# Kernel optimization log

Hardware: AMD Instinct MI355X
Metric: run time of the kernel (lower is better)

Reference implementation:

```python
import jax, jax.numpy as jnp
import numpy as np

B, N, C = 1, 768, 384
H, P = 12, 4
DP = 128  # dim_pair
HP3 = H * P * 3  # 144


def linear(x, W, b):
    # torch nn.Linear: y = x @ W.T + b, W shape (out, in)
    return jnp.einsum('...i,oi->...o', x, W) + b


def setup_inputs() -> dict:
    key = jax.random.key(0)
    ks = jax.random.split(key, 24)
    w = lambda k, *s: jax.random.normal(k, s, jnp.float32) * 0.02
    inp = {
        'single': jax.random.normal(ks[0], (B, N, C), jnp.float32),
        'pair': jax.random.normal(ks[1], (B, N, N, DP), jnp.float32),
        'rot': jax.random.normal(ks[2], (B, N, 3, 3), jnp.float32),
        'trans': jax.random.normal(ks[3], (B, N, 3), jnp.float32),
        'Wq': w(ks[4], C, C), 'bq': jnp.zeros((C,), jnp.float32),
        'Wk': w(ks[5], C, C), 'bk': jnp.zeros((C,), jnp.float32),
        'Wv': w(ks[6], C, C), 'bv': jnp.zeros((C,), jnp.float32),
        'Wpb': w(ks[7], H, DP), 'bpb': jnp.zeros((H,), jnp.float32),
        'Wqp': w(ks[8], HP3, C), 'bqp': jnp.zeros((HP3,), jnp.float32),
        'Wkp': w(ks[9], HP3, C), 'bkp': jnp.zeros((HP3,), jnp.float32),
        'Wvp': w(ks[10], HP3, C), 'bvp': jnp.zeros((HP3,), jnp.float32),
        'Wo': w(ks[11], C, C), 'bo': jnp.zeros((C,), jnp.float32),
        'Wpo': w(ks[12], C, HP3), 'bpo': jnp.zeros((C,), jnp.float32),
        'ln_w': jnp.ones((C,), jnp.float32), 'ln_b': jnp.zeros((C,), jnp.float32),
    }
    return inp


def reference(single, pair, rot, trans, Wq, bq, Wk, bk, Wv, bv, Wpb, bpb,
              Wqp, bqp, Wkp, bkp, Wvp, bvp, Wo, bo, Wpo, bpo, ln_w, ln_b):
    Ch = C // H
    scale = Ch ** -0.5
    q = linear(single, Wq, bq).reshape(B, N, H, Ch)
    k = linear(single, Wk, bk).reshape(B, N, H, Ch)
    v = linear(single, Wv, bv).reshape(B, N, H, Ch)
    pair_bias = jnp.transpose(linear(pair, Wpb, bpb), (0, 3, 1, 2))  # (B,H,N,N)

    q_pts = linear(single, Wqp, bqp).reshape(B, N, H, P, 3)
    k_pts = linear(single, Wkp, bkp).reshape(B, N, H, P, 3)
    v_pts = linear(single, Wvp, bvp).reshape(B, N, H, P, 3)
    t = trans[:, :, None, None, :]  # (B,N,1,1,3)
    # rotate local points into global frame: p @ R + t
    q_g = jnp.einsum('bnhpd,bnde->bnhpe', q_pts, rot) + t
    k_g = jnp.einsum('bnhpd,bnde->bnhpe', k_pts, rot) + t
    v_g = jnp.einsum('bnhpd,bnde->bnhpe', v_pts, rot) + t

    q2 = jnp.sum(q_g ** 2, axis=(3, 4))  # (B,N,H)
    k2 = jnp.sum(k_g ** 2, axis=(3, 4))
    qk = jnp.einsum('bnhpd,bmhpd->bhnm', q_g, k_g)
    q2h = jnp.transpose(q2, (0, 2, 1))  # (B,H,N)
    k2h = jnp.transpose(k2, (0, 2, 1))
    point_logits = -0.5 * (q2h[..., :, None] + k2h[..., None, :] - 2.0 * qk) * scale
    scalar_logits = jnp.einsum('bnhc,bmhc->bhnm', q, k) * scale
    attn = jax.nn.softmax(scalar_logits + pair_bias + point_logits, axis=-1)

    weighted_scalar = jnp.einsum('bhnm,bmhc->bnhc', attn, v).reshape(B, N, C)
    weighted_points = jnp.einsum('bhnm,bmhpd->bnhpd', attn, v_g).reshape(B, N, HP3)
    point_proj = linear(weighted_points, Wpo, bpo)
    out = linear(weighted_scalar + point_proj, Wo, bo)

    x = single + out
    mu = jnp.mean(x, axis=-1, keepdims=True)
    var = jnp.mean((x - mu) ** 2, axis=-1, keepdims=True)
    return (x - mu) / jnp.sqrt(var + 1e-5) * ln_w + ln_b
```

## Files before the change

### kernel.cpp

```cpp
#include <hip/hip_runtime.h>
#include <math.h>

#define NRES 768
#define CDIM 384
#define HEADS 12
#define SCALE 0.17677669529663687f

typedef _Float16 f16;
typedef _Float16 __attribute__((ext_vector_type(8))) f16x8;
typedef float __attribute__((ext_vector_type(4))) f32x4;

__global__ __launch_bounds__(256) void prep_kernel(
    const float* __restrict__ Wq, const float* __restrict__ Wk, const float* __restrict__ Wv,
    const float* __restrict__ Wqp, const float* __restrict__ Wkp, const float* __restrict__ Wvp,
    const float* __restrict__ bq, const float* __restrict__ bk, const float* __restrict__ bv,
    const float* __restrict__ bqp, const float* __restrict__ bkp, const float* __restrict__ bvp,
    const float* __restrict__ single, const float* __restrict__ Wpo, const float* __restrict__ bpo,
    const float* __restrict__ Wo,
    f16* __restrict__ WcatH, float* __restrict__ bcatP, f16* __restrict__ singleH,
    f16* __restrict__ WpoTE, f16* __restrict__ Bcat, f16* __restrict__ attn_cat) {
  int i = blockIdx.x * 256 + threadIdx.x;
  if (i < 614400) {
    int o = i / 384, c = i % 384;
    float v = 0.f;
    if (o < 384)       v = Wq[o * 384 + c];
    else if (o < 768)  v = Wk[(o - 384) * 384 + c];
    else if (o < 1152) v = Wv[(o - 768) * 384 + c];
    else if (o < 1296) v = Wqp[(o - 1152) * 384 + c];
    else if (o < 1440) v = Wkp[(o - 1296) * 384 + c];
    else if (o < 1584) v = Wvp[(o - 1440) * 384 + c];
    WcatH[i] = (f16)v;
    return;
  }
  i -= 614400;
  if (i < 1600) {
    float v = 0.f;
    if (i < 384)       v = bq[i];
    else if (i < 768)  v = bk[i - 384];
    else if (i < 1152) v = bv[i - 768];
    else if (i < 1296) v = bqp[i - 1152];
    else if (i < 1440) v = bkp[i - 1296];
    else if (i < 1584) v = bvp[i - 1440];
    bcatP[i] = v;
    return;
  }
  i -= 1600;
  if (i < 294912) { singleH[i] = (f16)single[i]; return; }
  i -= 294912;
  if (i < 73728) {
    int pr = i / 384, o = i % 384;
    float v = 0.f;
    if (pr < 144)       v = Wpo[o * 144 + pr];
    else if (pr == 144) v = bpo[o];
    WpoTE[i] = (f16)v;
    return;
  }
  i -= 73728;
  if (i < 147456) {
    int j = i / 384, k = i % 384;
    Bcat[(size_t)j * 576 + k] = (f16)Wo[j * 384 + k];
    return;
  }
  i -= 147456;
  if (i < 36864) {
    int n = i / 48, c = 528 + i % 48;
    attn_cat[(size_t)n * 576 + c] = (f16)(c == 528 ? 1.f : 0.f);
  }
}

__device__ __forceinline__ void gemm_tile(
    f16 (*As)[64], f16 (*Bs)[64],
    const f16* __restrict__ A, const f16* __restrict__ B,
    const float* __restrict__ bias, const float* __restrict__ res,
    float* __restrict__ Cf, f16* __restrict__ Ch,
    int Nd, int K, int lda, int ldb, int ldc, int bm, int bn) {
  const int t = threadIdx.x;
  const int w = t >> 6, l = t & 63;
  const int lg = l >> 4, lr = l & 15;
  f32x4 acc[4] = {{0.f,0.f,0.f,0.f},{0.f,0.f,0.f,0.f},{0.f,0.f,0.f,0.f},{0.f,0.f,0.f,0.f}};
  for (int k0 = 0; k0 < K; k0 += 64) {
    __syncthreads();
#pragma unroll
    for (int cc = 0; cc < 2; ++cc) {
      int c = t + cc * 256;
      int row = c >> 3, k8 = c & 7;
      int sw = (k8 ^ (row & 7)) * 8;
      *(f16x8*)&As[row][sw] = *(const f16x8*)(A + (size_t)(bm + row) * lda + k0 + k8 * 8);
      *(f16x8*)&Bs[row][sw] = *(const f16x8*)(B + (size_t)(bn + row) * ldb + k0 + k8 * 8);
    }
    __syncthreads();
#pragma unroll
    for (int ks = 0; ks < 2; ++ks) {
      f16x8 af = *(const f16x8*)&As[w * 16 + lr][((ks * 4 + lg) ^ (lr & 7)) * 8];
#pragma unroll
      for (int c = 0; c < 4; ++c) {
        f16x8 bf = *(const f16x8*)&Bs[c * 16 + lr][((ks * 4 + lg) ^ (lr & 7)) * 8];
        acc[c] = __builtin_amdgcn_mfma_f32_16x16x32_f16(af, bf, acc[c], 0, 0, 0);
      }
    }
  }
#pragma unroll
  for (int c = 0; c < 4; ++c) {
    int col = bn + c * 16 + lr;
    if (col >= Nd) continue;
    float bv = bias ? bias[col] : 0.f;
#pragma unroll
    for (int r = 0; r < 4; ++r) {
      int row = bm + w * 16 + lg * 4 + r;
      float v = acc[c][r] + bv;
      if (res) v += res[(size_t)row * ldc + col];
      if (Cf) Cf[(size_t)row * ldc + col] = v;
      else    Ch[(size_t)row * ldc + col] = (f16)v;
    }
  }
}

__global__ __launch_bounds__(256) void mega_gemm(
    const f16* __restrict__ singleH, const f16* __restrict__ WcatH,
    const float* __restrict__ bcatP, const f16* __restrict__ WpoTE,
    f16* __restrict__ Bcat, float* __restrict__ S) {
  __shared__ f16 As[64][64];
  __shared__ f16 Bs[64][64];
  const int bx = blockIdx.x, by = blockIdx.y;
  if (bx < 25) {
    gemm_tile(As, Bs, singleH, WcatH, bcatP, nullptr, S, nullptr,
              1584, 384, 384, 384, 1584, by * 64, bx * 64);
  } else if (by < 6) {
    gemm_tile(As, Bs, Bcat, WpoTE, nullptr, nullptr, nullptr, Bcat + 384,
              192, 384, 576, 384, 576, by * 64, (bx - 25) * 64);
  }
}

__global__ __launch_bounds__(256) void final_gemm(
    const f16* __restrict__ attn_cat, const f16* __restrict__ Bcat,
    const float* __restrict__ bo, const float* __restrict__ single,
    float* __restrict__ xb) {
  __shared__ f16 As[64][64];
  __shared__ f16 Bs[64][64];
  gemm_tile(As, Bs, attn_cat, Bcat, bo, single, xb, nullptr,
            384, 576, 576, 576, 384, blockIdx.y * 64, blockIdx.x * 64);
}

__global__ __launch_bounds__(256) void rot_feats2(
    const float* __restrict__ S, const float* __restrict__ rot, const float* __restrict__ trans,
    f16* __restrict__ qf, f16* __restrict__ kf, f16* __restrict__ vfT) {
  const int n = blockIdx.x * 256 + threadIdx.x;
  const int h = blockIdx.y;
  const float* Sr = S + (size_t)n * 1584;
  float R[9], T[3];
#pragma unroll
  for (int i = 0; i < 9; ++i) R[i] = rot[n * 9 + i];
#pragma unroll
  for (int i = 0; i < 3; ++i) T[i] = trans[n * 3 + i];
  float qv[64], kv[64];
#pragma unroll
  for (int c = 0; c < 32; ++c) {
    qv[c] = SCALE * Sr[h * 32 + c];
    kv[c] = Sr[384 + h * 32 + c];
    vfT[((size_t)(h * 48 + c)) * NRES + n] = (f16)Sr[768 + h * 32 + c];
  }
  float q2 = 0.f, k2 = 0.f;
#pragma unroll
  for (int p = 0; p < 4; ++p) {
    const float* qp = Sr + 1152 + (h * 4 + p) * 3;
    const float* kp = Sr + 1296 + (h * 4 + p) * 3;
    const float* vp = Sr + 1440 + (h * 4 + p) * 3;
#pragma unroll
    for (int e = 0; e < 3; ++e) {
      float qg = qp[0] * R[e] + qp[1] * R[3 + e] + qp[2] * R[6 + e] + T[e];
      float kg = kp[0] * R[e] + kp[1] * R[3 + e] + kp[2] * R[6 + e] + T[e];
      float vg = vp[0] * R[e] + vp[1] * R[3 + e] + vp[2] * R[6 + e] + T[e];
      qv[32 + p * 3 + e] = SCALE * qg; q2 += qg * qg;
      kv[32 + p * 3 + e] = kg;         k2 += kg * kg;
      vfT[((size_t)(h * 48 + 32 + p * 3 + e)) * NRES + n] = (f16)vg;
    }
  }
  qv[44] = -0.5f * SCALE * q2; qv[45] = 1.f;
  kv[44] = 1.f;                kv[45] = -0.5f * SCALE * k2;
#pragma unroll
  for (int c = 46; c < 64; ++c) { qv[c] = 0.f; kv[c] = 0.f; }
#pragma unroll
  for (int c = 44; c < 48; ++c) vfT[((size_t)(h * 48 + c)) * NRES + n] = (f16)0.f;
  f16* qo = qf + ((size_t)(h * NRES + n)) * 64;
  f16* ko = kf + ((size_t)(h * NRES + n)) * 64;
#pragma unroll
  for (int c = 0; c < 64; ++c) { qo[c] = (f16)qv[c]; ko[c] = (f16)kv[c]; }
}

__global__ __launch_bounds__(512) void fused_attn(
    const float* __restrict__ pair, const float* __restrict__ Wpb, const float* __restrict__ bpb,
    const f16* __restrict__ qf, const f16* __restrict__ kf, const f16* __restrict__ vfT,
    f16* __restrict__ partNh, float* __restrict__ partD) {
  __shared__ f16 bias_l[12 * 1160];
  __shared__ f16 p_l[8][1160];
  const int t = threadIdx.x;
  const int w = t >> 6, l = t & 63;
  const int lg = l >> 4, lr = l & 15;
  const int mblk = blockIdx.x;
  const int q0 = blockIdx.y * 16;
  const int m0 = mblk * 64;

  f16x8 bfr[4];
#pragma unroll
  for (int ks = 0; ks < 4; ++ks)
#pragma unroll
    for (int j = 0; j < 8; ++j)
      bfr[ks][j] = (f16)((lr < HEADS) ? Wpb[lr * 128 + ks * 32 + lg * 8 + j] : 0.f);
  const float bh = (lr < HEADS) ? bpb[lr] : 0.f;

#pragma unroll
  for (int g8 = 0; g8 < 8; ++g8) {
    const int g = w * 8 + g8;
    const int rowf = g * 16 + lr;
    const int nf = rowf >> 6, mf = rowf & 63;
    const float* ap = pair + (((size_t)(q0 + nf)) * NRES + (m0 + mf)) * 128 + lg * 8;
    f32x4 acc = {0.f, 0.f, 0.f, 0.f};
#pragma unroll
    for (int ks = 0; ks < 4; ++ks) {
      float4 a0 = *(const float4*)(ap + ks * 32);
      float4 a1 = *(const float4*)(ap + ks * 32 + 4);
      f16x8 af = {(f16)a0.x, (f16)a0.y, (f16)a0.z, (f16)a0.w,
                  (f16)a1.x, (f16)a1.y, (f16)a1.z, (f16)a1.w};
      acc = __builtin_amdgcn_mfma_f32_16x16x32_f16(af, bfr[ks], acc, 0, 0, 0);
    }
    if (lr < HEADS) {
#pragma unroll
      for (int r = 0; r < 4; ++r) {
        int rowo = g * 16 + lg * 4 + r;
        bias_l[lr * 1160 + (rowo >> 6) * 72 + (rowo & 63)] = (f16)(acc[r] + bh);
      }
    }
  }
  __syncthreads();

  for (int h = w; h < 12; h += 8) {
    const f16* qrow = qf + ((size_t)(h * NRES + q0 + lr)) * 64;
    f16x8 qa0 = *(const f16x8*)(qrow + lg * 8);
    f16x8 qa1 = *(const f16x8*)(qrow + 32 + lg * 8);
    float den[4] = {0.f, 0.f, 0.f, 0.f};
#pragma unroll
    for (int mc = 0; mc < 4; ++mc) {
      const f16* krow = kf + ((size_t)(h * NRES + m0 + mc * 16 + lr)) * 64;
      f16x8 kb0 = *(const f16x8*)(krow + lg * 8);
      f16x8 kb1 = *(const f16x8*)(krow + 32 + lg * 8);
      f32x4 s = {0.f, 0.f, 0.f, 0.f};
      s = __builtin_amdgcn_mfma_f32_16x16x32_f16(qa0, kb0, s, 0, 0, 0);
      s = __builtin_amdgcn_mfma_f32_16x16x32_f16(qa1, kb1, s, 0, 0, 0);
#pragma unroll
      for (int r = 0; r < 4; ++r) {
        float b = (float)bias_l[h * 1160 + (lg * 4 + r) * 72 + mc * 16 + lr];
        float e = __expf(s[r] + b);
        den[r] += e;
        p_l[w][(lg * 4 + r) * 72 + mc * 16 + lr] = (f16)e;
      }
    }
#pragma unroll
    for (int r = 0; r < 4; ++r) {
      float d = den[r];
      d += __shfl_xor(d, 1); d += __shfl_xor(d, 2);
      d += __shfl_xor(d, 4); d += __shfl_xor(d, 8);
      if (lr == 0)
        partD[((size_t)mblk * NRES + q0 + lg * 4 + r) * 12 + h] = d;
    }
#pragma unroll
    for (int c3 = 0; c3 < 3; ++c3) {
      f32x4 a = {0.f, 0.f, 0.f, 0.f};
#pragma unroll
      for (int ks = 0; ks < 2; ++ks) {
        f16x8 pa = *(const f16x8*)&p_l[w][lr * 72 + ks * 32 + lg * 8];
        f16x8 vb = *(const f16x8*)(vfT + ((size_t)(h * 48 + c3 * 16 + lr)) * NRES + m0 + ks * 32 + lg * 8);
        a = __builtin_amdgcn_mfma_f32_16x16x32_f16(pa, vb, a, 0, 0, 0);
      }
#pragma unroll
      for (int r = 0; r < 4; ++r)
        partNh[((size_t)mblk * NRES + q0 + lg * 4 + r) * 576 + h * 48 + c3 * 16 + lr] = (f16)a[r];
    }
  }
}

__global__ __launch_bounds__(576) void attn_reduce(
    const f16* __restrict__ partNh, const float* __restrict__ partD,
    f16* __restrict__ attn_cat) {
  const int n = blockIdx.x;
  const int hc = threadIdx.x;
  const int h = hc / 48, c = hc - h * 48;
  float num = 0.f, den = 0.f;
#pragma unroll
  for (int mc = 0; mc < 12; ++mc) {
    num += (float)partNh[((size_t)mc * NRES + n) * 576 + hc];
    den += partD[((size_t)mc * NRES + n) * 12 + h];
  }
  float val = num / den;
  if (c < 32)      attn_cat[(size_t)n * 576 + h * 32 + c] = (f16)val;
  else if (c < 44) attn_cat[(size_t)n * 576 + 384 + h * 12 + (c - 32)] = (f16)val;
}

__global__ __launch_bounds__(64) void ln_kernel(
    const float* __restrict__ x, const float* __restrict__ w, const float* __restrict__ b,
    float* __restrict__ out) {
  int n = blockIdx.x;
  int l = threadIdx.x;
  const float* xr = x + (size_t)n * CDIM;
  float v[6];
  float s = 0.f;
#pragma unroll
  for (int i = 0; i < 6; ++i) { v[i] = xr[l + 64 * i]; s += v[i]; }
#pragma unroll
  for (int o = 32; o; o >>= 1) s += __shfl_xor(s, o);
  float mu = s * (1.f / 384.f);
  float vs = 0.f;
#pragma unroll
  for (int i = 0; i < 6; ++i) { float d = v[i] - mu; vs += d * d; }
#pragma unroll
  for (int o = 32; o; o >>= 1) vs += __shfl_xor(vs, o);
  float rstd = rsqrtf(vs * (1.f / 384.f) + 1e-5f);
  float* orow = out + (size_t)n * CDIM;
#pragma unroll
  for (int i = 0; i < 6; ++i) {
    int c = l + 64 * i;
    orow[c] = (v[i] - mu) * rstd * w[c] + b[c];
  }
}

extern "C" void kernel_launch(void* const* d_in, const int* in_sizes, int n_in,
                              void* d_out, int out_size, void* d_ws, size_t ws_size,
                              hipStream_t stream) {
  const float* single = (const float*)d_in[0];
  const float* pair   = (const float*)d_in[1];
  const float* rot    = (const float*)d_in[2];
  const float* trans  = (const float*)d_in[3];
  const float* Wq  = (const float*)d_in[4];
  const float* bq  = (const float*)d_in[5];
  const float* Wk  = (const float*)d_in[6];
  const float* bk  = (const float*)d_in[7];
  const float* Wv  = (const float*)d_in[8];
  const float* bv  = (const float*)d_in[9];
  const float* Wpb = (const float*)d_in[10];
  const float* bpb = (const float*)d_in[11];
  const float* Wqp = (const float*)d_in[12];
  const float* bqp = (const float*)d_in[13];
  const float* Wkp = (const float*)d_in[14];
  const float* bkp = (const float*)d_in[15];
  const float* Wvp = (const float*)d_in[16];
  const float* bvp = (const float*)d_in[17];
  const float* Wo  = (const float*)d_in[18];
  const float* bo  = (const float*)d_in[19];
  const float* Wpo = (const float*)d_in[20];
  const float* bpo = (const float*)d_in[21];
  const float* lnw = (const float*)d_in[22];
  const float* lnb = (const float*)d_in[23];

  float* ws = (float*)d_ws;
  f16* WcatH    = (f16*)ws; ws += 1600 * 384 / 2;
  float* bcatP  = ws;       ws += 1600;
  f16* singleH  = (f16*)ws; ws += 768 * 384 / 2;
  f16* WpoTE    = (f16*)ws; ws += 192 * 384 / 2;
  f16* Bcat     = (f16*)ws; ws += 384 * 576 / 2;
  float* S      = ws;       ws += 768 * 1584;
  f16* qf       = (f16*)ws; ws += 12 * 768 * 64 / 2;
  f16* kf       = (f16*)ws; ws += 12 * 768 * 64 / 2;
  f16* vfT      = (f16*)ws; ws += 12 * 48 * 768 / 2;
  f16* partNh   = (f16*)ws; ws += 12 * 768 * 576 / 2;
  float* partD  = ws;       ws += 12 * 768 * 12;
  f16* attn_cat = (f16*)ws; ws += 768 * 576 / 2;
  float* xb     = ws;       ws += 768 * 384;

  prep_kernel<<<4567, 256, 0, stream>>>(Wq, Wk, Wv, Wqp, Wkp, Wvp,
                                        bq, bk, bv, bqp, bkp, bvp,
                                        single, Wpo, bpo, Wo,
                                        WcatH, bcatP, singleH, WpoTE, Bcat, attn_cat);
  mega_gemm<<<dim3(28, 12), 256, 0, stream>>>(singleH, WcatH, bcatP, WpoTE, Bcat, S);
  rot_feats2<<<dim3(3, 12), 256, 0, stream>>>(S, rot, trans, qf, kf, vfT);
  fused_attn<<<dim3(12, 48), 512, 0, stream>>>(pair, Wpb, bpb, qf, kf, vfT, partNh, partD);
  attn_reduce<<<768, 576, 0, stream>>>(partNh, partD, attn_cat);
  final_gemm<<<dim3(6, 12), 256, 0, stream>>>(attn_cat, Bcat, bo, single, xb);
  ln_kernel<<<768, 64, 0, stream>>>(xb, lnw, lnb, (float*)d_out);
}
```

Measured before the change: 139.4 us.

## Fuse fp16 weight/input conversion into GEMM loads and drop prep kernel

Removes the separate prep kernel by converting fp32 weights and activations to fp16 inside the GEMM tile loads, selecting source matrices per row on the fly. The projection output S is stored as fp16 instead of fp32, and rot_feats reads it with vector loads and writes vectorized q/k features. The combined Wo·Wpo matrix is written to its own buffer, and final_gemm reads Wo directly. The constant columns of attn_cat are now written in attn_reduce. This saves a launch and an intermediate round trip through memory, at the cost of extra conversion work repeated in each tile, strided Wpo gathers, and reduced precision in S.

Measured after the change: 135.4 us. 2.9% less time.

```diff
diff --git a/kernel.cpp b/kernel.cpp
--- a/kernel.cpp
+++ b/kernel.cpp
@@ -10,181 +10,220 @@
 typedef _Float16 __attribute__((ext_vector_type(8))) f16x8;
 typedef float __attribute__((ext_vector_type(4))) f32x4;
 
-__global__ __launch_bounds__(256) void prep_kernel(
+__device__ __forceinline__ f16x8 ldcvt8(const float* __restrict__ p) {
+  float4 a = *(const float4*)p;
+  float4 b = *(const float4*)(p + 4);
+  f16x8 r = {(f16)a.x, (f16)a.y, (f16)a.z, (f16)a.w,
+             (f16)b.x, (f16)b.y, (f16)b.z, (f16)b.w};
+  return r;
+}
+
+__device__ __forceinline__ void mfma_step(f16 (*As)[64], f16 (*Bs)[64],
+                                          int w, int lg, int lr, f32x4* acc) {
+#pragma unroll
+  for (int ks = 0; ks < 2; ++ks) {
+    f16x8 af = *(const f16x8*)&As[w * 16 + lr][((ks * 4 + lg) ^ (lr & 7)) * 8];
+#pragma unroll
+    for (int c = 0; c < 4; ++c) {
+      f16x8 bf = *(const f16x8*)&Bs[c * 16 + lr][((ks * 4 + lg) ^ (lr & 7)) * 8];
+      acc[c] = __builtin_amdgcn_mfma_f32_16x16x32_f16(af, bf, acc[c], 0, 0, 0);
+    }
+  }
+}
+
+__global__ __launch_bounds__(256) void mega_gemm(
+    const float* __restrict__ single,
     const float* __restrict__ Wq, const float* __restrict__ Wk, const float* __restrict__ Wv,
     const float* __restrict__ Wqp, const float* __restrict__ Wkp, const float* __restrict__ Wvp,
     const float* __restrict__ bq, const float* __restrict__ bk, const float* __restrict__ bv,
     const float* __restrict__ bqp, const float* __restrict__ bkp, const float* __restrict__ bvp,
-    const float* __restrict__ single, const float* __restrict__ Wpo, const float* __restrict__ bpo,
-    const float* __restrict__ Wo,
-    f16* __restrict__ WcatH, float* __restrict__ bcatP, f16* __restrict__ singleH,
-    f16* __restrict__ WpoTE, f16* __restrict__ Bcat, f16* __restrict__ attn_cat) {
-  int i = blockIdx.x * 256 + threadIdx.x;
-  if (i < 614400) {
-    int o = i / 384, c = i % 384;
-    float v = 0.f;
-    if (o < 384)       v = Wq[o * 384 + c];
-    else if (o < 768)  v = Wk[(o - 384) * 384 + c];
-    else if (o < 1152) v = Wv[(o - 768) * 384 + c];
-    else if (o < 1296) v = Wqp[(o - 1152) * 384 + c];
-    else if (o < 1440) v = Wkp[(o - 1296) * 384 + c];
-    else if (o < 1584) v = Wvp[(o - 1440) * 384 + c];
-    WcatH[i] = (f16)v;
-    return;
-  }
-  i -= 614400;
-  if (i < 1600) {
-    float v = 0.f;
-    if (i < 384)       v = bq[i];
-    else if (i < 768)  v = bk[i - 384];
-    else if (i < 1152) v = bv[i - 768];
-    else if (i < 1296) v = bqp[i - 1152];
-    else if (i < 1440) v = bkp[i - 1296];
-    else if (i < 1584) v = bvp[i - 1440];
-    bcatP[i] = v;
-    return;
-  }
-  i -= 1600;
-  if (i < 294912) { singleH[i] = (f16)single[i]; return; }
-  i -= 294912;
-  if (i < 73728) {
-    int pr = i / 384, o = i % 384;
-    float v = 0.f;
-    if (pr < 144)       v = Wpo[o * 144 + pr];
-    else if (pr == 144) v = bpo[o];
-    WpoTE[i] = (f16)v;
-    return;
-  }
-  i -= 73728;
-  if (i < 147456) {
-    int j = i / 384, k = i % 384;
-    Bcat[(size_t)j * 576 + k] = (f16)Wo[j * 384 + k];
-    return;
-  }
-  i -= 147456;
-  if (i < 36864) {
-    int n = i / 48, c = 528 + i % 48;
-    attn_cat[(size_t)n * 576 + c] = (f16)(c == 528 ? 1.f : 0.f);
-  }
-}
-
-__device__ __forceinline__ void gemm_tile(
-    f16 (*As)[64], f16 (*Bs)[64],
-    const f16* __restrict__ A, const f16* __restrict__ B,
-    const float* __restrict__ bias, const float* __restrict__ res,
-    float* __restrict__ Cf, f16* __restrict__ Ch,
-    int Nd, int K, int lda, int ldb, int ldc, int bm, int bn) {
+    const float* __restrict__ Wpo, const float* __restrict__ bpo, const float* __restrict__ Wo,
+    f16* __restrict__ Wcomb, f16* __restrict__ S16) {
+  __shared__ f16 As[64][64];
+  __shared__ f16 Bs[64][64];
+  const int bx = blockIdx.x, by = blockIdx.y;
   const int t = threadIdx.x;
   const int w = t >> 6, l = t & 63;
   const int lg = l >> 4, lr = l & 15;
+  const f16 z0 = (f16)0.f;
   f32x4 acc[4] = {{0.f,0.f,0.f,0.f},{0.f,0.f,0.f,0.f},{0.f,0.f,0.f,0.f},{0.f,0.f,0.f,0.f}};
-  for (int k0 = 0; k0 < K; k0 += 64) {
+
+  if (bx < 25) {
+    const int bm = by * 64, bn = bx * 64;
+    for (int k0 = 0; k0 < 384; k0 += 64) {
+      __syncthreads();
+#pragma unroll
+      for (int cc = 0; cc < 2; ++cc) {
+        int c = t + cc * 256;
+        int row = c >> 3, k8 = c & 7;
+        int sw = (k8 ^ (row & 7)) * 8;
+        *(f16x8*)&As[row][sw] = ldcvt8(single + (size_t)(bm + row) * 384 + k0 + k8 * 8);
+        int o = bn + row;
+        const float* bsrc;
+        if (o < 384)       bsrc = Wq  + (size_t)o * 384;
+        else if (o < 768)  bsrc = Wk  + (size_t)(o - 384) * 384;
+        else if (o < 1152) bsrc = Wv  + (size_t)(o - 768) * 384;
+        else if (o < 1296) bsrc = Wqp + (size_t)(o - 1152) * 384;
+        else if (o < 1440) bsrc = Wkp + (size_t)(o - 1296) * 384;
+        else if (o < 1584) bsrc = Wvp + (size_t)(o - 1440) * 384;
+        else               bsrc = nullptr;
+        f16x8 vb8 = {z0, z0, z0, z0, z0, z0, z0, z0};
+        if (bsrc) vb8 = ldcvt8(bsrc + k0 + k8 * 8);
+        *(f16x8*)&Bs[row][sw] = vb8;
+      }
+      __syncthreads();
+      mfma_step(As, Bs, w, lg, lr, acc);
+    }
+#pragma unroll
+    for (int c = 0; c < 4; ++c) {
+      int col = bn + c * 16 + lr;
+      if (col >= 1584) continue;
+      float bb;
+      if (col < 384)       bb = bq[col];
+      else if (col < 768)  bb = bk[col - 384];
+      else if (col < 1152) bb = bv[col - 768];
+      else if (col < 1296) bb = bqp[col - 1152];
+      else if (col < 1440) bb = bkp[col - 1296];
+      else                 bb = bvp[col - 1440];
+#pragma unroll
+      for (int r = 0; r < 4; ++r) {
+        int row = bm + w * 16 + lg * 4 + r;
+        S16[(size_t)row * 1584 + col] = (f16)(acc[c][r] + bb);
+      }
+    }
+  } else if (by < 6) {
+    const int bm = by * 64, bn = (bx - 25) * 64;
+    for (int k0 = 0; k0 < 384; k0 += 64) {
+      __syncthreads();
+#pragma unroll
+      for (int cc = 0; cc < 2; ++cc) {
+        int c = t + cc * 256;
+        int row = c >> 3, k8 = c & 7;
+        int sw = (k8 ^ (row & 7)) * 8;
+        *(f16x8*)&As[row][sw] = ldcvt8(Wo + (size_t)(bm + row) * 384 + k0 + k8 * 8);
+        int pr = bn + row;
+        f16x8 vb8 = {z0, z0, z0, z0, z0, z0, z0, z0};
+        if (pr < 144) {
+#pragma unroll
+          for (int j = 0; j < 8; ++j) vb8[j] = (f16)Wpo[(size_t)(k0 + k8 * 8 + j) * 144 + pr];
+        } else if (pr == 144) {
+#pragma unroll
+          for (int j = 0; j < 8; ++j) vb8[j] = (f16)bpo[k0 + k8 * 8 + j];
+        }
+        *(f16x8*)&Bs[row][sw] = vb8;
+      }
+      __syncthreads();
+      mfma_step(As, Bs, w, lg, lr, acc);
+    }
+#pragma unroll
+    for (int c = 0; c < 4; ++c) {
+      int col = bn + c * 16 + lr;
+      if (col >= 192) continue;
+#pragma unroll
+      for (int r = 0; r < 4; ++r)
+        Wcomb[(size_t)(bm + w * 16 + lg * 4 + r) * 192 + col] = (f16)acc[c][r];
+    }
+  }
+}
+
+__global__ __launch_bounds__(256) void final_gemm(
+    const f16* __restrict__ attn_cat, const float* __restrict__ Wo,
+    const f16* __restrict__ Wcomb, const float* __restrict__ bo,
+    const float* __restrict__ single, float* __restrict__ xb) {
+  __shared__ f16 As[64][64];
+  __shared__ f16 Bs[64][64];
+  const int t = threadIdx.x;
+  const int w = t >> 6, l = t & 63;
+  const int lg = l >> 4, lr = l & 15;
+  const int bm = blockIdx.y * 64, bn = blockIdx.x * 64;
+  f32x4 acc[4] = {{0.f,0.f,0.f,0.f},{0.f,0.f,0.f,0.f},{0.f,0.f,0.f,0.f},{0.f,0.f,0.f,0.f}};
+  for (int k0 = 0; k0 < 576; k0 += 64) {
     __syncthreads();
 #pragma unroll
     for (int cc = 0; cc < 2; ++cc) {
       int c = t + cc * 256;
       int row = c >> 3, k8 = c & 7;
       int sw = (k8 ^ (row & 7)) * 8;
-      *(f16x8*)&As[row][sw] = *(const f16x8*)(A + (size_t)(bm + row) * lda + k0 + k8 * 8);
-      *(f16x8*)&Bs[row][sw] = *(const f16x8*)(B + (size_t)(bn + row) * ldb + k0 + k8 * 8);
+      *(f16x8*)&As[row][sw] = *(const f16x8*)(attn_cat + (size_t)(bm + row) * 576 + k0 + k8 * 8);
+      f16x8 vb8;
+      if (k0 < 384) vb8 = ldcvt8(Wo + (size_t)(bn + row) * 384 + k0 + k8 * 8);
+      else          vb8 = *(const f16x8*)(Wcomb + (size_t)(bn + row) * 192 + (k0 - 384) + k8 * 8);
+      *(f16x8*)&Bs[row][sw] = vb8;
     }
     __syncthreads();
-#pragma unroll
-    for (int ks = 0; ks < 2; ++ks) {
-      f16x8 af = *(const f16x8*)&As[w * 16 + lr][((ks * 4 + lg) ^ (lr & 7)) * 8];
-#pragma unroll
-      for (int c = 0; c < 4; ++c) {
-        f16x8 bf = *(const f16x8*)&Bs[c * 16 + lr][((ks * 4 + lg) ^ (lr & 7)) * 8];
-        acc[c] = __builtin_amdgcn_mfma_f32_16x16x32_f16(af, bf, acc[c], 0, 0, 0);
-      }
-    }
+    mfma_step(As, Bs, w, lg, lr, acc);
   }
 #pragma unroll
   for (int c = 0; c < 4; ++c) {
     int col = bn + c * 16 + lr;
-    if (col >= Nd) continue;
-    float bv = bias ? bias[col] : 0.f;
+    float bb = bo[col];
 #pragma unroll
     for (int r = 0; r < 4; ++r) {
       int row = bm + w * 16 + lg * 4 + r;
-      float v = acc[c][r] + bv;
-      if (res) v += res[(size_t)row * ldc + col];
-      if (Cf) Cf[(size_t)row * ldc + col] = v;
-      else    Ch[(size_t)row * ldc + col] = (f16)v;
-    }
-  }
-}
-
-__global__ __launch_bounds__(256) void mega_gemm(
-    const f16* __restrict__ singleH, const f16* __restrict__ WcatH,
-    const float* __restrict__ bcatP, const f16* __restrict__ WpoTE,
-    f16* __restrict__ Bcat, float* __restrict__ S) {
-  __shared__ f16 As[64][64];
-  __shared__ f16 Bs[64][64];
-  const int bx = blockIdx.x, by = blockIdx.y;
-  if (bx < 25) {
-    gemm_tile(As, Bs, singleH, WcatH, bcatP, nullptr, S, nullptr,
-              1584, 384, 384, 384, 1584, by * 64, bx * 64);
-  } else if (by < 6) {
-    gemm_tile(As, Bs, Bcat, WpoTE, nullptr, nullptr, nullptr, Bcat + 384,
-              192, 384, 576, 384, 576, by * 64, (bx - 25) * 64);
-  }
-}
-
-__global__ __launch_bounds__(256) void final_gemm(
-    const f16* __restrict__ attn_cat, const f16* __restrict__ Bcat,
-    const float* __restrict__ bo, const float* __restrict__ single,
-    float* __restrict__ xb) {
-  __shared__ f16 As[64][64];
-  __shared__ f16 Bs[64][64];
-  gemm_tile(As, Bs, attn_cat, Bcat, bo, single, xb, nullptr,
-            384, 576, 576, 576, 384, blockIdx.y * 64, blockIdx.x * 64);
-}
-
-__global__ __launch_bounds__(256) void rot_feats2(
-    const float* __restrict__ S, const float* __restrict__ rot, const float* __restrict__ trans,
+      xb[(size_t)row * 384 + col] = acc[c][r] + bb + single[(size_t)row * 384 + col];
+    }
+  }
+}
+
+__global__ __launch_bounds__(256) void rot_feats3(
+    const f16* __restrict__ S16, const float* __restrict__ rot, const float* __restrict__ trans,
     f16* __restrict__ qf, f16* __restrict__ kf, f16* __restrict__ vfT) {
   const int n = blockIdx.x * 256 + threadIdx.x;
   const int h = blockIdx.y;
-  const float* Sr = S + (size_t)n * 1584;
+  const f16* Sr = S16 + (size_t)n * 1584;
   float R[9], T[3];
 #pragma unroll
   for (int i = 0; i < 9; ++i) R[i] = rot[n * 9 + i];
 #pragma unroll
   for (int i = 0; i < 3; ++i) T[i] = trans[n * 3 + i];
-  float qv[64], kv[64];
+  f16 qh[64], kh[64];
+  f16x8 qv4[4], kv4[4], vv4[4];
+#pragma unroll
+  for (int j = 0; j < 4; ++j) {
+    qv4[j] = *(const f16x8*)(Sr + h * 32 + j * 8);
+    kv4[j] = *(const f16x8*)(Sr + 384 + h * 32 + j * 8);
+    vv4[j] = *(const f16x8*)(Sr + 768 + h * 32 + j * 8);
+  }
 #pragma unroll
   for (int c = 0; c < 32; ++c) {
-    qv[c] = SCALE * Sr[h * 32 + c];
-    kv[c] = Sr[384 + h * 32 + c];
-    vfT[((size_t)(h * 48 + c)) * NRES + n] = (f16)Sr[768 + h * 32 + c];
+    qh[c] = (f16)(SCALE * (float)qv4[c >> 3][c & 7]);
+    vfT[((size_t)(h * 48 + c)) * NRES + n] = vv4[c >> 3][c & 7];
+  }
+#pragma unroll
+  for (int j = 0; j < 4; ++j) *(f16x8*)&kh[j * 8] = kv4[j];
+  float qp[12], kp[12], vp[12];
+#pragma unroll
+  for (int e = 0; e < 12; ++e) {
+    qp[e] = (float)Sr[1152 + h * 12 + e];
+    kp[e] = (float)Sr[1296 + h * 12 + e];
+    vp[e] = (float)Sr[1440 + h * 12 + e];
   }
   float q2 = 0.f, k2 = 0.f;
 #pragma unroll
   for (int p = 0; p < 4; ++p) {
-    const float* qp = Sr + 1152 + (h * 4 + p) * 3;
-    const float* kp = Sr + 1296 + (h * 4 + p) * 3;
-    const float* vp = Sr + 1440 + (h * 4 + p) * 3;
 #pragma unroll
     for (int e = 0; e < 3; ++e) {
-      float qg = qp[0] * R[e] + qp[1] * R[3 + e] + qp[2] * R[6 + e] + T[e];
-      float kg = kp[0] * R[e] + kp[1] * R[3 + e] + kp[2] * R[6 + e] + T[e];
-      float vg = vp[0] * R[e] + vp[1] * R[3 + e] + vp[2] * R[6 + e] + T[e];
-      qv[32 + p * 3 + e] = SCALE * qg; q2 += qg * qg;
-      kv[32 + p * 3 + e] = kg;         k2 += kg * kg;
-      vfT[((size_t)(h * 48 + 32 + p * 3 + e)) * NRES + n] = (f16)vg;
-    }
-  }
-  qv[44] = -0.5f * SCALE * q2; qv[45] = 1.f;
-  kv[44] = 1.f;                kv[45] = -0.5f * SCALE * k2;
-#pragma unroll
-  for (int c = 46; c < 64; ++c) { qv[c] = 0.f; kv[c] = 0.f; }
+      float qg = qp[p*3+0] * R[e] + qp[p*3+1] * R[3+e] + qp[p*3+2] * R[6+e] + T[e];
+      float kg = kp[p*3+0] * R[e] + kp[p*3+1] * R[3+e] + kp[p*3+2] * R[6+e] + T[e];
+      float vg = vp[p*3+0] * R[e] + vp[p*3+1] * R[3+e] + vp[p*3+2] * R[6+e] + T[e];
+      qh[32 + p*3 + e] = (f16)(SCALE * qg); q2 += qg * qg;
+      kh[32 + p*3 + e] = (f16)kg;           k2 += kg * kg;
+      vfT[((size_t)(h * 48 + 32 + p*3 + e)) * NRES + n] = (f16)vg;
+    }
+  }
+  qh[44] = (f16)(-0.5f * SCALE * q2); qh[45] = (f16)1.f;
+  kh[44] = (f16)1.f;                  kh[45] = (f16)(-0.5f * SCALE * k2);
+#pragma unroll
+  for (int c = 46; c < 64; ++c) { qh[c] = (f16)0.f; kh[c] = (f16)0.f; }
 #pragma unroll
   for (int c = 44; c < 48; ++c) vfT[((size_t)(h * 48 + c)) * NRES + n] = (f16)0.f;
   f16* qo = qf + ((size_t)(h * NRES + n)) * 64;
   f16* ko = kf + ((size_t)(h * NRES + n)) * 64;
 #pragma unroll
-  for (int c = 0; c < 64; ++c) { qo[c] = (f16)qv[c]; ko[c] = (f16)kv[c]; }
+  for (int j = 0; j < 8; ++j) {
+    *(f16x8*)&qo[j * 8] = *(const f16x8*)&qh[j * 8];
+    *(f16x8*)&ko[j * 8] = *(const f16x8*)&kh[j * 8];
+  }
 }
 
 __global__ __launch_bounds__(512) void fused_attn(
@@ -293,6 +332,7 @@
   float val = num / den;
   if (c < 32)      attn_cat[(size_t)n * 576 + h * 32 + c] = (f16)val;
   else if (c < 44) attn_cat[(size_t)n * 576 + 384 + h * 12 + (c - 32)] = (f16)val;
+  if (hc < 48)     attn_cat[(size_t)n * 576 + 528 + hc] = (f16)(hc == 0 ? 1.f : 0.f);
 }
 
 __global__ __launch_bounds__(64) void ln_kernel(
@@ -351,12 +391,8 @@
   const float* lnb = (const float*)d_in[23];
 
   float* ws = (float*)d_ws;
-  f16* WcatH    = (f16*)ws; ws += 1600 * 384 / 2;
-  float* bcatP  = ws;       ws += 1600;
-  f16* singleH  = (f16*)ws; ws += 768 * 384 / 2;
-  f16* WpoTE    = (f16*)ws; ws += 192 * 384 / 2;
-  f16* Bcat     = (f16*)ws; ws += 384 * 576 / 2;
-  float* S      = ws;       ws += 768 * 1584;
+  f16* S16      = (f16*)ws; ws += 768 * 1584 / 2;
+  f16* Wcomb    = (f16*)ws; ws += 384 * 192 / 2;
   f16* qf       = (f16*)ws; ws += 12 * 768 * 64 / 2;
   f16* kf       = (f16*)ws; ws += 12 * 768 * 64 / 2;
   f16* vfT      = (f16*)ws; ws += 12 * 48 * 768 / 2;
@@ -365,14 +401,13 @@
   f16* attn_cat = (f16*)ws; ws += 768 * 576 / 2;
   float* xb     = ws;       ws += 768 * 384;
 
-  prep_kernel<<<4567, 256, 0, stream>>>(Wq, Wk, Wv, Wqp, Wkp, Wvp,
-                                        bq, bk, bv, bqp, bkp, bvp,
-                                        single, Wpo, bpo, Wo,
-                                        WcatH, bcatP, singleH, WpoTE, Bcat, attn_cat);
-  mega_gemm<<<dim3(28, 12), 256, 0, stream>>>(singleH, WcatH, bcatP, WpoTE, Bcat, S);
-  rot_feats2<<<dim3(3, 12), 256, 0, stream>>>(S, rot, trans, qf, kf, vfT);
+  mega_gemm<<<dim3(28, 12), 256, 0, stream>>>(single,
+                                              Wq, Wk, Wv, Wqp, Wkp, Wvp,
+                                              bq, bk, bv, bqp, bkp, bvp,
+                                              Wpo, bpo, Wo, Wcomb, S16);
+  rot_feats3<<<dim3(3, 12), 256, 0, stream>>>(S16, rot, trans, qf, kf, vfT);
   fused_attn<<<dim3(12, 48), 512, 0, stream>>>(pair, Wpb, bpb, qf, kf, vfT, partNh, partD);
   attn_reduce<<<768, 576, 0, stream>>>(partNh, partD, attn_cat);
-  final_gemm<<<dim3(6, 12), 256, 0, stream>>>(attn_cat, Bcat, bo, single, xb);
+  final_gemm<<<dim3(6, 12), 256, 0, stream>>>(attn_cat, Wo, Wcomb, bo, single, xb);
   ln_kernel<<<768, 64, 0, stream>>>(xb, lnw, lnb, (float*)d_out);
 }
```
